# Performance work log

Hardware: AMD Instinct MI355X
Metric: run time of the kernel (lower is better)

Reference implementation:

```python
import jax, jax.numpy as jnp
import numpy as np

B, S, HID = 1, 2048, 4096
H = 32
Q_LORA, KV_LORA = 1536, 512
NOPE, ROPE, VDIM = 128, 64, 128
EPS = 1e-6
ROPE_BASE = 10000.0


def rms_norm(x, w, eps=EPS):
    var = jnp.mean(x.astype(jnp.float32) ** 2, axis=-1, keepdims=True)
    return (x * jax.lax.rsqrt(var + eps)).astype(x.dtype) * w


def rope_cos_sin(position_ids, dim=ROPE):
    inv_freq = 1.0 / (ROPE_BASE ** (jnp.arange(0, dim, 2, dtype=jnp.float32) / dim))
    ang = position_ids.astype(jnp.float32)[..., None] * inv_freq  # [B,S,dim/2]
    return jnp.cos(ang), jnp.sin(ang)


def apply_rope(x, cos, sin):
    # x: [..., dim]; neox-style rotate_half on the rope slice
    d2 = x.shape[-1] // 2
    x1, x2 = x[..., :d2], x[..., d2:]
    return jnp.concatenate([x1 * cos - x2 * sin, x2 * cos + x1 * sin], axis=-1)


def setup_inputs() -> dict:
    key = jax.random.key(0)
    ks = jax.random.split(key, 8)
    s = 0.02
    return {
        "position_ids": jnp.broadcast_to(jnp.arange(S, dtype=jnp.int32), (B, S)),
        "hidden_states": jax.random.normal(ks[0], (B, S, HID), jnp.float32),
        "w_fused_a": jax.random.normal(ks[1], (Q_LORA + KV_LORA + ROPE, HID), jnp.float32) * s,
        "q_a_ln_w": jnp.ones((Q_LORA,), jnp.float32),
        "kv_a_ln_w": jnp.ones((KV_LORA,), jnp.float32),
        "w_q_b": jax.random.normal(ks[2], (H * (NOPE + ROPE), Q_LORA), jnp.float32) * s,
        "w_kv_b": jax.random.normal(ks[3], (H * 2 * NOPE, KV_LORA), jnp.float32) * s,
        "w_o": jax.random.normal(ks[4], (HID, H * VDIM), jnp.float32) * s,
    }


def reference(position_ids, hidden_states, w_fused_a, q_a_ln_w, kv_a_ln_w, w_q_b, w_kv_b, w_o):
    # fused A projection: -> [q_lora | kv_lora | rope]
    a = jnp.einsum('bsh,oh->bso', hidden_states, w_fused_a)
    cq = rms_norm(a[..., :Q_LORA], q_a_ln_w)
    ckv = rms_norm(a[..., Q_LORA:Q_LORA + KV_LORA], kv_a_ln_w)
    k_pe = a[..., Q_LORA + KV_LORA:]  # [B,S,ROPE], shared across heads

    # Q up-projection, split nope/rope per head
    q = jnp.einsum('bsr,or->bso', cq, w_q_b).reshape(B, S, H, NOPE + ROPE)
    q_nope, q_pe = q[..., :NOPE], q[..., NOPE:]

    # KV up-projection: per head [k_nope | v]
    kv = jnp.einsum('bsr,or->bso', ckv, w_kv_b).reshape(B, S, H, 2 * NOPE)
    k_nope, v = kv[..., :NOPE], kv[..., NOPE:]

    # RoPE on the rope slices only
    cos, sin = rope_cos_sin(position_ids)  # [B,S,ROPE/2]
    q_pe = apply_rope(q_pe, cos[:, :, None, :], sin[:, :, None, :])
    k_pe = apply_rope(k_pe, cos, sin)

    qf = jnp.concatenate([q_nope, q_pe], axis=-1)  # [B,S,H,NOPE+ROPE]
    kf = jnp.concatenate([k_nope, jnp.broadcast_to(k_pe[:, :, None, :], (B, S, H, ROPE))], axis=-1)

    scale = 1.0 / np.sqrt(NOPE + ROPE)
    scores = jnp.einsum('bshd,bthd->bhst', qf, kf) * scale
    causal = jnp.tril(jnp.ones((S, S), dtype=bool))
    scores = jnp.where(causal, scores, jnp.finfo(scores.dtype).min)
    p = jax.nn.softmax(scores, axis=-1)
    attn = jnp.einsum('bhst,bthd->bshd', p, v).reshape(B, S, H * VDIM)
    return jnp.einsum('bsd,od->bso', attn, w_o)
```

## Files before the change

kernel.cpp:

```cpp
#include <hip/hip_runtime.h>
#include <cmath>

#define S_LEN 2048
#define HID 4096
#define NHEAD 32
#define Q_LORA 1536
#define KV_LORA 512
#define NOPE 128
#define ROPE_D 64
#define VDIM 128
#define QK_DIM 192
#define FUSED_N 2112
#define FUSED_NPAD 2304

typedef __attribute__((ext_vector_type(8))) short short8;
typedef __attribute__((ext_vector_type(4))) float floatx4;
typedef unsigned short ushort_t;

__device__ inline short f2bf(float f) {
    union { float f; unsigned u; } v; v.f = f;
    unsigned r = (v.u + 0x7fffu + ((v.u >> 16) & 1u)) >> 16;
    return (short)r;
}
__device__ inline float bf2f(ushort_t u) {
    union { unsigned u; float f; } v; v.u = ((unsigned)u) << 16; return v.f;
}

#define GLOAD16(g, l)                                                        \
    __builtin_amdgcn_global_load_lds(                                        \
        (const __attribute__((address_space(1))) unsigned int*)(g),          \
        (__attribute__((address_space(3))) unsigned int*)(l), 16, 0, 0)

__device__ inline short8 conv8(const float* s) {
    const float4* s4 = (const float4*)s;
    float4 a = s4[0], b = s4[1];
    short8 v;
    v[0] = f2bf(a.x); v[1] = f2bf(a.y); v[2] = f2bf(a.z); v[3] = f2bf(a.w);
    v[4] = f2bf(b.x); v[5] = f2bf(b.y); v[6] = f2bf(b.z); v[7] = f2bf(b.w);
    return v;
}

#define CE0 (S_LEN * HID)
#define CE1 (CE0 + FUSED_NPAD * HID)
#define CE2 (CE1 + NHEAD * QK_DIM * Q_LORA)
#define CE3 (CE2 + NHEAD * 256 * KV_LORA)

__global__ __launch_bounds__(256) void conv_all(
    const float* __restrict__ hs, const float* __restrict__ w_a,
    const float* __restrict__ w_qb, const float* __restrict__ w_kvb,
    ushort_t* __restrict__ hs_bf, ushort_t* __restrict__ w_a_bf,
    ushort_t* __restrict__ w_qb_bf, ushort_t* __restrict__ w_kvb_bf)
{
    int i = (blockIdx.x * 256 + threadIdx.x) * 8;
    if (i < CE0) {
        *(short8*)(hs_bf + i) = conv8(hs + i);
    } else if (i < CE1) {
        int j = i - CE0;
        short8 v;
        if (j < FUSED_N * HID) v = conv8(w_a + j);
        else                   v = (short8){0,0,0,0,0,0,0,0};
        *(short8*)(w_a_bf + j) = v;
    } else if (i < CE2) {
        int j = i - CE1;
        *(short8*)(w_qb_bf + j) = conv8(w_qb + j);
    } else if (i < CE3) {
        int j = i - CE2;
        *(short8*)(w_kvb_bf + j) = conv8(w_kvb + j);
    }
}

__global__ __launch_bounds__(256) void conv_bf16(
    const float* __restrict__ src, ushort_t* __restrict__ dst, int n)
{
    int i = (blockIdx.x * 256 + threadIdx.x) * 8;
    if (i >= n) return;
    *(short8*)(dst + i) = conv8(src + i);
}

__global__ __launch_bounds__(256) void reduce_add_f32(
    const float* __restrict__ p0, const float* __restrict__ p1,
    float* __restrict__ o, int n)
{
    int i = (blockIdx.x * 256 + threadIdx.x) * 4;
    if (i >= n) return;
    float4 a = *(const float4*)(p0 + i);
    float4 b = *(const float4*)(p1 + i);
    float4 c; c.x = a.x + b.x; c.y = a.y + b.y; c.z = a.z + b.z; c.w = a.w + b.w;
    *(float4*)(o + i) = c;
}

__device__ __forceinline__ void gemm_pipe_body(
    const ushort_t* __restrict__ A, int lda,
    const ushort_t* __restrict__ B, int ldb,
    int m0, int n0, int kbeg, int nst,
    short8* LDS, floatx4 (&acc)[8][4], int tid)
{
    const int lane = tid & 63;
    const int wave = tid >> 6;
    const int m    = lane & 15;
    const int quad = lane >> 4;
    const int wr   = wave >> 2;
    const int wc   = wave & 3;

    auto stage = [&](int k0, int buf) {
        short8* dst = &LDS[buf * 2048];
        #pragma unroll
        for (int r = 0; r < 2; ++r) {
            int i  = tid + r * 512;
            int mi = i & 15, qd = (i >> 4) & 3, rb = i >> 6;
            GLOAD16(A + (size_t)(m0 + rb * 16 + mi) * lda + k0 + qd * 8, dst + i);
            GLOAD16(B + (size_t)(n0 + rb * 16 + mi) * ldb + k0 + qd * 8, dst + 1024 + i);
        }
    };

    stage(kbeg, 0);
    stage(kbeg + 32, 1);

    for (int i = 0; i < nst; ++i) {
        if (i + 2 < nst) {
            stage(kbeg + (i + 2) * 32, (i + 2) % 3);
            asm volatile("s_waitcnt vmcnt(8)" ::: "memory");
        } else if (i + 1 < nst) {
            asm volatile("s_waitcnt vmcnt(4)" ::: "memory");
        } else {
            asm volatile("s_waitcnt vmcnt(0)" ::: "memory");
        }
        asm volatile("s_barrier" ::: "memory");

        const short8* As = &LDS[(i % 3) * 2048];
        const short8* Bs = As + 1024;
        short8 af[8], bfr[4];
        #pragma unroll
        for (int ii = 0; ii < 8; ++ii)
            af[ii] = As[((wr * 8 + ii) * 4 + quad) * 16 + m];
        #pragma unroll
        for (int j = 0; j < 4; ++j)
            bfr[j] = Bs[((wc * 4 + j) * 4 + quad) * 16 + m];

        __builtin_amdgcn_s_setprio(1);
        #pragma unroll
        for (int ri = 0; ri < 8; ++ri)
            #pragma unroll
            for (int ci = 0; ci < 4; ++ci)
                acc[ri][ci] = __builtin_amdgcn_mfma_f32_16x16x32_bf16(
                    af[ri], bfr[ci], acc[ri][ci], 0, 0, 0);
        __builtin_amdgcn_s_setprio(0);

        asm volatile("s_barrier" ::: "memory");
    }
}

__device__ inline void store_c(float* p, float v)    { *p = v; }
__device__ inline void store_c(ushort_t* p, float v) { *p = (ushort_t)f2bf(v); }

template <typename CT>
__device__ __forceinline__ void gemm256_store(
    CT* __restrict__ C, int ldc, int N, int m0, int n0,
    floatx4 (&acc)[8][4], int tid)
{
    const int lane = tid & 63;
    const int wave = tid >> 6;
    const int m    = lane & 15;
    const int quad = lane >> 4;
    const int wr   = wave >> 2, wc = wave & 3;
    #pragma unroll
    for (int ci = 0; ci < 4; ++ci) {
        int col = n0 + wc * 64 + ci * 16 + m;
        if (col < N) {
            #pragma unroll
            for (int ri = 0; ri < 8; ++ri) {
                int row = m0 + wr * 128 + ri * 16 + quad * 4;
                #pragma unroll
                for (int r = 0; r < 4; ++r)
                    store_c(&C[(size_t)(row + r) * ldc + col], acc[ri][ci][r]);
            }
        }
    }
}

template <typename CT>
__global__ __launch_bounds__(512) void gemm256p(
    const ushort_t* __restrict__ A, int lda,
    const ushort_t* __restrict__ B, int ldb,
    CT* __restrict__ C, int ldc, int N, int Klen, int nx, int ny)
{
    __shared__ short8 LDS[3 * 2048];
    const int tid = threadIdx.x;

    const int nwg = gridDim.x;
    const int bid = blockIdx.x;
    const int wg  = (bid & 7) * (nwg >> 3) + (bid >> 3);
    const int nxy = nx * ny;
    const int z   = wg / nxy;
    const int rxy = wg - z * nxy;
    const int m0  = (rxy / nx) * 256;
    const int n0  = (rxy % nx) * 256;
    CT* Cz = C + (size_t)z * (size_t)ny * 256 * ldc;

    floatx4 acc[8][4];
    #pragma unroll
    for (int i = 0; i < 8; ++i)
        #pragma unroll
        for (int j = 0; j < 4; ++j) acc[i][j] = (floatx4){0.f, 0.f, 0.f, 0.f};

    gemm_pipe_body(A, lda, B, ldb, m0, n0, z * Klen, Klen >> 5, LDS, acc, tid);
    gemm256_store<CT>(Cz, ldc, N, m0, n0, acc, tid);
}

__global__ __launch_bounds__(512) void gemm34p(
    const ushort_t* __restrict__ a_bf,
    const ushort_t* __restrict__ w_qb_bf,
    const ushort_t* __restrict__ w_kvb_bf,
    ushort_t* __restrict__ q_bf,
    ushort_t* __restrict__ kv_bf)
{
    __shared__ short8 LDS[3 * 2048];
    const int tid = threadIdx.x;

    const int nwg = gridDim.x;
    const int bid = blockIdx.x;
    const int wg  = (bid & 7) * (nwg >> 3) + (bid >> 3);
    const int x   = wg % 56;
    const int m0  = (wg / 56) * 256;

    const ushort_t* A; const ushort_t* B; ushort_t* C;
    int ldb, ldc, N, K, n0;
    if (x < 24) {
        A = a_bf;            B = w_qb_bf;  C = q_bf;
        ldb = Q_LORA;        ldc = NHEAD * QK_DIM; N = NHEAD * QK_DIM;
        K = Q_LORA;          n0 = x * 256;
    } else {
        A = a_bf + Q_LORA;   B = w_kvb_bf; C = kv_bf;
        ldb = KV_LORA;       ldc = NHEAD * 256;    N = NHEAD * 256;
        K = KV_LORA;         n0 = (x - 24) * 256;
    }

    floatx4 acc[8][4];
    #pragma unroll
    for (int i = 0; i < 8; ++i)
        #pragma unroll
        for (int j = 0; j < 4; ++j) acc[i][j] = (floatx4){0.f, 0.f, 0.f, 0.f};

    gemm_pipe_body(A, FUSED_N, B, ldb, m0, n0, 0, K >> 5, LDS, acc, tid);
    gemm256_store<ushort_t>(C, ldc, N, m0, n0, acc, tid);
}

__global__ __launch_bounds__(256) void norm_rope_kernel(
    const float* __restrict__ part,
    ushort_t* __restrict__ a,
    const float* __restrict__ q_ln_w,
    const float* __restrict__ kv_ln_w,
    const int* __restrict__ pos_ids)
{
    const int s = blockIdx.x;
    const size_t PL = (size_t)S_LEN * FUSED_N;
    const float* r0 = part + (size_t)s * FUSED_N;
    ushort_t* row = a + (size_t)s * FUSED_N;
    __shared__ float red[256];
    const int tid = threadIdx.x;

    float vq[6];
    float ss = 0.f;
    #pragma unroll
    for (int j = 0; j < 6; ++j) {
        int i = tid + j * 256;
        vq[j] = (r0[i] + r0[i + PL]) + (r0[i + 2 * PL] + r0[i + 3 * PL]);
        ss += vq[j] * vq[j];
    }
    red[tid] = ss;
    __syncthreads();
    for (int w = 128; w > 0; w >>= 1) {
        if (tid < w) red[tid] += red[tid + w];
        __syncthreads();
    }
    float scale_q = rsqrtf(red[0] / (float)Q_LORA + 1e-6f);
    #pragma unroll
    for (int j = 0; j < 6; ++j) {
        int i = tid + j * 256;
        row[i] = (ushort_t)f2bf(vq[j] * scale_q * q_ln_w[i]);
    }
    __syncthreads();

    float vk[2];
    ss = 0.f;
    #pragma unroll
    for (int j = 0; j < 2; ++j) {
        int iw = tid + j * 256;
        int i  = Q_LORA + iw;
        vk[j] = (r0[i] + r0[i + PL]) + (r0[i + 2 * PL] + r0[i + 3 * PL]);
        ss += vk[j] * vk[j];
    }
    red[tid] = ss;
    __syncthreads();
    for (int w = 128; w > 0; w >>= 1) {
        if (tid < w) red[tid] += red[tid + w];
        __syncthreads();
    }
    float scale_kv = rsqrtf(red[0] / (float)KV_LORA + 1e-6f);
    #pragma unroll
    for (int j = 0; j < 2; ++j) {
        int iw = tid + j * 256;
        row[Q_LORA + iw] = (ushort_t)f2bf(vk[j] * scale_kv * kv_ln_w[iw]);
    }

    if (tid < 32) {
        const int j = tid;
        float pos = (float)pos_ids[s];
        float inv_freq = expf(-(float)j * (9.210340371976184f / 32.f));
        float ang = pos * inv_freq;
        float c = cosf(ang), sn = sinf(ang);
        int i1 = Q_LORA + KV_LORA + j;
        int i2 = i1 + 32;
        float x1 = (r0[i1] + r0[i1 + PL]) + (r0[i1 + 2 * PL] + r0[i1 + 3 * PL]);
        float x2 = (r0[i2] + r0[i2 + PL]) + (r0[i2 + 2 * PL] + r0[i2 + 3 * PL]);
        row[i1] = (ushort_t)f2bf(x1 * c - x2 * sn);
        row[i2] = (ushort_t)f2bf(x2 * c + x1 * sn);
    }
}

__global__ __launch_bounds__(256) void rope_q_kernel(
    ushort_t* __restrict__ q, const int* __restrict__ pos_ids)
{
    int idx = blockIdx.x * blockDim.x + threadIdx.x;
    if (idx >= S_LEN * NHEAD) return;
    int s = idx >> 5;
    float pos = (float)pos_ids[s];
    ushort_t* qp = q + (size_t)idx * QK_DIM + NOPE;
    #pragma unroll 4
    for (int j = 0; j < 32; ++j) {
        float inv_freq = expf(-(float)j * (9.210340371976184f / 32.f));
        float ang = pos * inv_freq;
        float c = cosf(ang), sn = sinf(ang);
        float x1 = bf2f(qp[j]), x2 = bf2f(qp[32 + j]);
        qp[j]      = (ushort_t)f2bf(x1 * c - x2 * sn);
        qp[32 + j] = (ushort_t)f2bf(x2 * c + x1 * sn);
    }
}

__global__ __launch_bounds__(256) void transpose_v(
    const ushort_t* __restrict__ kv, ushort_t* __restrict__ vt)
{
    __shared__ ushort_t vs[32][128];
    const int tid = threadIdx.x;
    const int h   = blockIdx.y;
    const int kb  = blockIdx.x;

    #pragma unroll
    for (int rep = 0; rep < 2; ++rep) {
        int i = rep * 256 + tid;
        int key = i >> 4, ch = i & 15;
        *(short8*)&vs[key][ch * 8] =
            *(const short8*)(kv + ((size_t)(kb * 32 + key) * NHEAD + h) * 256 + 128 + ch * 8);
    }
    __syncthreads();
    #pragma unroll
    for (int rep = 0; rep < 2; ++rep) {
        int i = rep * 256 + tid;
        int kq = i >> 7, d = i & 127;
        short8 v;
        #pragma unroll
        for (int j = 0; j < 8; ++j) v[j] = vs[kq * 8 + j][d];
        *(short8*)(vt + (((size_t)h * (S_LEN / 8) + kb * 4 + kq) * 128 + d) * 8) = v;
    }
}

__global__ __launch_bounds__(256) void attn_mfma(
    const ushort_t* __restrict__ q,
    const ushort_t* __restrict__ kv,
    const ushort_t* __restrict__ abuf,
    const ushort_t* __restrict__ vt,
    ushort_t* __restrict__ attn)
{
    __shared__ short8 KF[3][768];
    __shared__ short8 VF[3][512];
    __shared__ short8 PA[256];

    const int tid  = threadIdx.x;
    const int wave = tid >> 6;
    const int lane = tid & 63;
    const int m    = lane & 15;
    const int quad = lane >> 4;
    const int h    = blockIdx.y;
    const int pair = blockIdx.x;
    const int qtiles[2] = { 31 - pair, pair };

    const float scale2 = 0.07216878364870323f * 1.4426950408889634f;
    short* pas = (short*)PA;

    auto stage_kv = [&](int t0, int buf) {
        #pragma unroll
        for (int rep = 0; rep < 3; ++rep) {
            int i   = rep * 256 + tid;
            int key = i & 31, qd = (i >> 5) & 3, c = i >> 7;
            if (c < 4)
                GLOAD16(kv + ((size_t)(t0 + key) * NHEAD + h) * 256 + c * 32 + qd * 8,
                        &KF[buf][i]);
            else
                GLOAD16(abuf + (size_t)(t0 + key) * FUSED_N + 2048 + (c - 4) * 32 + qd * 8,
                        &KF[buf][i]);
        }
        const ushort_t* vsrc = vt + ((size_t)h * (S_LEN / 8) + (t0 >> 3)) * 1024;
        GLOAD16(vsrc + (size_t)tid * 8, &VF[buf][tid]);
        GLOAD16(vsrc + (size_t)(256 + tid) * 8, &VF[buf][256 + tid]);
    };

    for (int qi = 0; qi < 2; ++qi) {
        const int q0 = qtiles[qi] * 64;
        const int qrow_base = q0 + wave * 16;

        short8 qf[6];
        {
            const ushort_t* qrow = q + ((size_t)(qrow_base + m) * NHEAD + h) * QK_DIM;
            #pragma unroll
            for (int c = 0; c < 6; ++c)
                qf[c] = *(const short8*)(qrow + c * 32 + quad * 8);
        }

        floatx4 O[8];
        #pragma unroll
        for (int t = 0; t < 8; ++t) O[t] = (floatx4){0.f, 0.f, 0.f, 0.f};
        float mrow[4] = {-1e30f, -1e30f, -1e30f, -1e30f};
        float lrow[4] = {0.f, 0.f, 0.f, 0.f};

        const int ntile = (q0 + 64) / 32;

        stage_kv(0, 0);
        stage_kv(32, 1);

        for (int tt = 0; tt < ntile; ++tt) {
            const int t0 = tt * 32;
            if (tt + 2 < ntile) {
                stage_kv(t0 + 64, (tt + 2) % 3);
                asm volatile("s_waitcnt vmcnt(10)" ::: "memory");
            } else if (tt + 1 < ntile) {
                asm volatile("s_waitcnt vmcnt(5)" ::: "memory");
            } else {
                asm volatile("s_waitcnt vmcnt(0)" ::: "memory");
            }
            asm volatile("s_barrier" ::: "memory");
            const int cur = tt % 3;

            floatx4 s0 = (floatx4){0.f, 0.f, 0.f, 0.f};
            floatx4 s1 = (floatx4){0.f, 0.f, 0.f, 0.f};
            const int kb = quad * 32 + m;
            __builtin_amdgcn_s_setprio(1);
            #pragma unroll
            for (int c = 0; c < 6; ++c) {
                s0 = __builtin_amdgcn_mfma_f32_16x16x32_bf16(qf[c], KF[cur][c * 128 + kb],      s0, 0, 0, 0);
                s1 = __builtin_amdgcn_mfma_f32_16x16x32_bf16(qf[c], KF[cur][c * 128 + kb + 16], s1, 0, 0, 0);
            }
            __builtin_amdgcn_s_setprio(0);

            const int qb = qrow_base + quad * 4;
            float sv0[4], sv1[4];
            #pragma unroll
            for (int r = 0; r < 4; ++r) {
                float a0 = s0[r] * scale2;
                float a1 = s1[r] * scale2;
                if (t0 + m > qb + r)      a0 = -1e30f;
                if (t0 + 16 + m > qb + r) a1 = -1e30f;
                sv0[r] = a0; sv1[r] = a1;
            }
            #pragma unroll
            for (int r = 0; r < 4; ++r) {
                float v = fmaxf(sv0[r], sv1[r]);
                if (!__all(v <= mrow[r] + 8.f)) {
                    v = fmaxf(v, __shfl_xor(v, 1));
                    v = fmaxf(v, __shfl_xor(v, 2));
                    v = fmaxf(v, __shfl_xor(v, 4));
                    v = fmaxf(v, __shfl_xor(v, 8));
                    float mnew  = fmaxf(mrow[r], v);
                    float alpha = exp2f(mrow[r] - mnew);
                    lrow[r] *= alpha;
                    #pragma unroll
                    for (int t = 0; t < 8; ++t) O[t][r] *= alpha;
                    mrow[r] = mnew;
                }
                float p0 = exp2f(sv0[r] - mrow[r]);
                float p1 = exp2f(sv1[r] - mrow[r]);
                lrow[r] += p0 + p1;
                int row = quad * 4 + r;
                short* pw = pas + wave * 512;
                pw[((m >> 3) + 0) * 128 + row * 8 + (m & 7)] = f2bf(p0);
                pw[((m >> 3) + 2) * 128 + row * 8 + (m & 7)] = f2bf(p1);
            }

            short8 pfrag = PA[wave * 64 + quad * 16 + m];
            __builtin_amdgcn_s_setprio(1);
            #pragma unroll
            for (int t = 0; t < 8; ++t) {
                O[t] = __builtin_amdgcn_mfma_f32_16x16x32_bf16(
                    pfrag, VF[cur][quad * 128 + m + 16 * t], O[t], 0, 0, 0);
            }
            __builtin_amdgcn_s_setprio(0);

            asm volatile("s_barrier" ::: "memory");
        }

        #pragma unroll
        for (int r = 0; r < 4; ++r) {
            float l = lrow[r];
            l += __shfl_xor(l, 1);
            l += __shfl_xor(l, 2);
            l += __shfl_xor(l, 4);
            l += __shfl_xor(l, 8);
            float linv = 1.f / l;
            int row = qrow_base + quad * 4 + r;
            ushort_t* dst = attn + ((size_t)row * NHEAD + h) * VDIM + m;
            #pragma unroll
            for (int t = 0; t < 8; ++t)
                dst[16 * t] = (ushort_t)f2bf(O[t][r] * linv);
        }
    }
}

extern "C" void kernel_launch(void* const* d_in, const int* in_sizes, int n_in,
                              void* d_out, int out_size, void* d_ws, size_t ws_size,
                              hipStream_t stream)
{
    const int*   pos    = (const int*)d_in[0];
    const float* hs     = (const float*)d_in[1];
    const float* w_a    = (const float*)d_in[2];
    const float* qlnw   = (const float*)d_in[3];
    const float* kvlnw  = (const float*)d_in[4];
    const float* w_qb   = (const float*)d_in[5];
    const float* w_kvb  = (const float*)d_in[6];
    const float* w_o    = (const float*)d_in[7];
    float* out = (float*)d_out;

    char* p = (char*)d_ws;
    ushort_t* a_bf    = (ushort_t*)p; p += (size_t)S_LEN * FUSED_N * 2;
    ushort_t* q_bf    = (ushort_t*)p; p += (size_t)S_LEN * NHEAD * QK_DIM * 2;
    ushort_t* kv_bf   = (ushort_t*)p; p += (size_t)S_LEN * NHEAD * 256 * 2;
    ushort_t* attn_bf = (ushort_t*)p; p += (size_t)S_LEN * HID * 2;
    ushort_t* hs_bf   = (ushort_t*)p; p += (size_t)S_LEN * HID * 2;
    ushort_t* w_a_bf  = (ushort_t*)p; p += (size_t)FUSED_NPAD * HID * 2;
    ushort_t* w_qb_bf = (ushort_t*)p; p += (size_t)NHEAD * QK_DIM * Q_LORA * 2;
    ushort_t* w_kvb_bf= (ushort_t*)p; p += (size_t)NHEAD * 256 * KV_LORA * 2;
    ushort_t* w_o_bf  = hs_bf;
    ushort_t* vt_bf   = w_qb_bf;
    float* part1 = (float*)q_bf;
    float* part7 = (float*)a_bf;

    if (ws_size < (size_t)(p - (char*)d_ws)) return;

    dim3 blk(256);
    dim3 blk512(512);
    auto cgrid = [](size_t n) { return dim3((unsigned)((n / 8 + 255) / 256)); };

    conv_all<<<dim3(CE3 / 2048), blk, 0, stream>>>(
        hs, w_a, w_qb, w_kvb, hs_bf, w_a_bf, w_qb_bf, w_kvb_bf);

    gemm256p<float><<<dim3((FUSED_NPAD / 256) * (S_LEN / 256) * 4), blk512, 0, stream>>>(
        hs_bf, HID, w_a_bf, HID, part1, FUSED_N, FUSED_N, HID / 4,
        FUSED_NPAD / 256, S_LEN / 256);

    conv_bf16<<<cgrid((size_t)HID * HID), blk, 0, stream>>>(w_o, w_o_bf, HID * HID);

    norm_rope_kernel<<<S_LEN, 256, 0, stream>>>(part1, a_bf, qlnw, kvlnw, pos);

    gemm34p<<<dim3(56 * (S_LEN / 256)), blk512, 0, stream>>>(
        a_bf, w_qb_bf, w_kvb_bf, q_bf, kv_bf);

    transpose_v<<<dim3(S_LEN / 32, NHEAD), blk, 0, stream>>>(kv_bf, vt_bf);

    rope_q_kernel<<<(S_LEN * NHEAD + 255) / 256, 256, 0, stream>>>(q_bf, pos);

    attn_mfma<<<dim3(16, NHEAD), blk, 0, stream>>>(
        q_bf, kv_bf, a_bf, vt_bf, attn_bf);

    gemm256p<float><<<dim3((HID / 256) * (S_LEN / 256) * 2), blk512, 0, stream>>>(
        attn_bf, HID, w_o_bf, HID, part7, HID, HID, HID / 2,
        HID / 256, S_LEN / 256);
    reduce_add_f32<<<cgrid((size_t)S_LEN * HID * 2), blk, 0, stream>>>(
        part7, part7 + (size_t)S_LEN * HID, out, S_LEN * HID);
}
```

Baseline: 622.8 us.

## Fuse V transpose into KV GEMM epilogue and drop trailing pipeline barriers

The KV up-projection epilogue now writes the V half directly into the transposed vt layout, which removes the separate transpose_v kernel and its extra global round trip. vt gets its own workspace buffer instead of aliasing the Q_B weight buffer. The GEMM pipeline moves to a 4-slot LDS ring while keeping a prefetch distance of two, so the trailing barrier per K step can be dropped. The attention kernel shortens its KV prefetch to distance one and removes its per-tile trailing barrier, adding one barrier per query block instead. Larger LDS use may lower occupancy, and the narrower short4 scattered stores for vt may be less efficient than the old staged transpose.

Result: faster. 590.7 us (-5.1%).

```diff
diff --git a/kernel.cpp b/kernel.cpp
--- a/kernel.cpp
+++ b/kernel.cpp
@@ -14,6 +14,7 @@
 #define FUSED_NPAD 2304
 
 typedef __attribute__((ext_vector_type(8))) short short8;
+typedef __attribute__((ext_vector_type(4))) short short4v;
 typedef __attribute__((ext_vector_type(4))) float floatx4;
 typedef unsigned short ushort_t;
 
@@ -118,7 +119,7 @@
 
     for (int i = 0; i < nst; ++i) {
         if (i + 2 < nst) {
-            stage(kbeg + (i + 2) * 32, (i + 2) % 3);
+            stage(kbeg + (i + 2) * 32, (i + 2) & 3);
             asm volatile("s_waitcnt vmcnt(8)" ::: "memory");
         } else if (i + 1 < nst) {
             asm volatile("s_waitcnt vmcnt(4)" ::: "memory");
@@ -127,7 +128,7 @@
         }
         asm volatile("s_barrier" ::: "memory");
 
-        const short8* As = &LDS[(i % 3) * 2048];
+        const short8* As = &LDS[(i & 3) * 2048];
         const short8* Bs = As + 1024;
         short8 af[8], bfr[4];
         #pragma unroll
@@ -145,8 +146,6 @@
                 acc[ri][ci] = __builtin_amdgcn_mfma_f32_16x16x32_bf16(
                     af[ri], bfr[ci], acc[ri][ci], 0, 0, 0);
         __builtin_amdgcn_s_setprio(0);
-
-        asm volatile("s_barrier" ::: "memory");
     }
 }
 
@@ -184,7 +183,7 @@
     const ushort_t* __restrict__ B, int ldb,
     CT* __restrict__ C, int ldc, int N, int Klen, int nx, int ny)
 {
-    __shared__ short8 LDS[3 * 2048];
+    __shared__ short8 LDS[4 * 2048];
     const int tid = threadIdx.x;
 
     const int nwg = gridDim.x;
@@ -212,9 +211,10 @@
     const ushort_t* __restrict__ w_qb_bf,
     const ushort_t* __restrict__ w_kvb_bf,
     ushort_t* __restrict__ q_bf,
-    ushort_t* __restrict__ kv_bf)
-{
-    __shared__ short8 LDS[3 * 2048];
+    ushort_t* __restrict__ kv_bf,
+    ushort_t* __restrict__ vt)
+{
+    __shared__ short8 LDS[4 * 2048];
     const int tid = threadIdx.x;
 
     const int nwg = gridDim.x;
@@ -223,16 +223,14 @@
     const int x   = wg % 56;
     const int m0  = (wg / 56) * 256;
 
-    const ushort_t* A; const ushort_t* B; ushort_t* C;
-    int ldb, ldc, N, K, n0;
+    const ushort_t* A; const ushort_t* B;
+    int ldb, K, n0;
     if (x < 24) {
-        A = a_bf;            B = w_qb_bf;  C = q_bf;
-        ldb = Q_LORA;        ldc = NHEAD * QK_DIM; N = NHEAD * QK_DIM;
-        K = Q_LORA;          n0 = x * 256;
+        A = a_bf;            B = w_qb_bf;
+        ldb = Q_LORA;        K = Q_LORA;   n0 = x * 256;
     } else {
-        A = a_bf + Q_LORA;   B = w_kvb_bf; C = kv_bf;
-        ldb = KV_LORA;       ldc = NHEAD * 256;    N = NHEAD * 256;
-        K = KV_LORA;         n0 = (x - 24) * 256;
+        A = a_bf + Q_LORA;   B = w_kvb_bf;
+        ldb = KV_LORA;       K = KV_LORA;  n0 = (x - 24) * 256;
     }
 
     floatx4 acc[8][4];
@@ -242,7 +240,43 @@
         for (int j = 0; j < 4; ++j) acc[i][j] = (floatx4){0.f, 0.f, 0.f, 0.f};
 
     gemm_pipe_body(A, FUSED_N, B, ldb, m0, n0, 0, K >> 5, LDS, acc, tid);
-    gemm256_store<ushort_t>(C, ldc, N, m0, n0, acc, tid);
+
+    const int lane = tid & 63;
+    const int wave = tid >> 6;
+    const int m    = lane & 15;
+    const int quad = lane >> 4;
+    const int wr   = wave >> 2, wc = wave & 3;
+
+    if (x < 24) {
+        gemm256_store<ushort_t>(q_bf, NHEAD * QK_DIM, NHEAD * QK_DIM, m0, n0, acc, tid);
+    } else {
+        const int h = x - 24;
+        #pragma unroll
+        for (int ci = 0; ci < 4; ++ci) {
+            int dd = wc * 64 + ci * 16 + m;
+            if (dd < 128) {
+                #pragma unroll
+                for (int ri = 0; ri < 8; ++ri) {
+                    int row = m0 + wr * 128 + ri * 16 + quad * 4;
+                    #pragma unroll
+                    for (int r = 0; r < 4; ++r)
+                        kv_bf[(size_t)(row + r) * (NHEAD * 256) + h * 256 + dd] =
+                            (ushort_t)f2bf(acc[ri][ci][r]);
+                }
+            } else {
+                int d = dd - 128;
+                #pragma unroll
+                for (int ri = 0; ri < 8; ++ri) {
+                    int row0 = m0 + wr * 128 + ri * 16 + quad * 4;
+                    short4v v4;
+                    #pragma unroll
+                    for (int r = 0; r < 4; ++r) v4[r] = f2bf(acc[ri][ci][r]);
+                    *(short4v*)(vt + (((size_t)h * (S_LEN / 8) + (row0 >> 3)) * 128 + d) * 8
+                                   + (row0 & 7)) = v4;
+                }
+            }
+        }
+    }
 }
 
 __global__ __launch_bounds__(256) void norm_rope_kernel(
@@ -337,33 +371,6 @@
     }
 }
 
-__global__ __launch_bounds__(256) void transpose_v(
-    const ushort_t* __restrict__ kv, ushort_t* __restrict__ vt)
-{
-    __shared__ ushort_t vs[32][128];
-    const int tid = threadIdx.x;
-    const int h   = blockIdx.y;
-    const int kb  = blockIdx.x;
-
-    #pragma unroll
-    for (int rep = 0; rep < 2; ++rep) {
-        int i = rep * 256 + tid;
-        int key = i >> 4, ch = i & 15;
-        *(short8*)&vs[key][ch * 8] =
-            *(const short8*)(kv + ((size_t)(kb * 32 + key) * NHEAD + h) * 256 + 128 + ch * 8);
-    }
-    __syncthreads();
-    #pragma unroll
-    for (int rep = 0; rep < 2; ++rep) {
-        int i = rep * 256 + tid;
-        int kq = i >> 7, d = i & 127;
-        short8 v;
-        #pragma unroll
-        for (int j = 0; j < 8; ++j) v[j] = vs[kq * 8 + j][d];
-        *(short8*)(vt + (((size_t)h * (S_LEN / 8) + kb * 4 + kq) * 128 + d) * 8) = v;
-    }
-}
-
 __global__ __launch_bounds__(256) void attn_mfma(
     const ushort_t* __restrict__ q,
     const ushort_t* __restrict__ kv,
@@ -425,14 +432,11 @@
         const int ntile = (q0 + 64) / 32;
 
         stage_kv(0, 0);
-        stage_kv(32, 1);
 
         for (int tt = 0; tt < ntile; ++tt) {
             const int t0 = tt * 32;
-            if (tt + 2 < ntile) {
-                stage_kv(t0 + 64, (tt + 2) % 3);
-                asm volatile("s_waitcnt vmcnt(10)" ::: "memory");
-            } else if (tt + 1 < ntile) {
+            if (tt + 1 < ntile) {
+                stage_kv(t0 + 32, (tt + 1) % 3);
                 asm volatile("s_waitcnt vmcnt(5)" ::: "memory");
             } else {
                 asm volatile("s_waitcnt vmcnt(0)" ::: "memory");
@@ -493,8 +497,6 @@
                     pfrag, VF[cur][quad * 128 + m + 16 * t], O[t], 0, 0, 0);
             }
             __builtin_amdgcn_s_setprio(0);
-
-            asm volatile("s_barrier" ::: "memory");
         }
 
         #pragma unroll
@@ -511,6 +513,7 @@
             for (int t = 0; t < 8; ++t)
                 dst[16 * t] = (ushort_t)f2bf(O[t][r] * linv);
         }
+        asm volatile("s_barrier" ::: "memory");
     }
 }
 
@@ -537,8 +540,8 @@
     ushort_t* w_a_bf  = (ushort_t*)p; p += (size_t)FUSED_NPAD * HID * 2;
     ushort_t* w_qb_bf = (ushort_t*)p; p += (size_t)NHEAD * QK_DIM * Q_LORA * 2;
     ushort_t* w_kvb_bf= (ushort_t*)p; p += (size_t)NHEAD * 256 * KV_LORA * 2;
+    ushort_t* vt_bf   = (ushort_t*)p; p += (size_t)S_LEN * HID * 2;
     ushort_t* w_o_bf  = hs_bf;
-    ushort_t* vt_bf   = w_qb_bf;
     float* part1 = (float*)q_bf;
     float* part7 = (float*)a_bf;
 
@@ -560,9 +563,7 @@
     norm_rope_kernel<<<S_LEN, 256, 0, stream>>>(part1, a_bf, qlnw, kvlnw, pos);
 
     gemm34p<<<dim3(56 * (S_LEN / 256)), blk512, 0, stream>>>(
-        a_bf, w_qb_bf, w_kvb_bf, q_bf, kv_bf);
-
-    transpose_v<<<dim3(S_LEN / 32, NHEAD), blk, 0, stream>>>(kv_bf, vt_bf);
+        a_bf, w_qb_bf, w_kvb_bf, q_bf, kv_bf, vt_bf);
 
     rope_q_kernel<<<(S_LEN * NHEAD + 255) / 256, 256, 0, stream>>>(q_bf, pos);
 
```
